# Kernel tuning notes

Hardware: AMD Instinct MI355X
Metric: run time of the kernel (lower is better)

Reference implementation:

```python
import jax, jax.numpy as jnp
import numpy as np
import math

B, S, HID = 2, 2048, 1024
NH, HD = 16, 64
MAX_SEQ = 65536  # RoPE base from RotaryEmbedding


def _rope_tables(seq_len, dim):
    inv_freq = 1.0 / (MAX_SEQ ** (jnp.arange(0, dim, 2, dtype=jnp.float32) / dim))
    t = jnp.arange(seq_len, dtype=jnp.float32)
    freqs = jnp.einsum('i,j->ij', t, inv_freq)          # [S, dim/2]
    emb = jnp.concatenate([freqs, freqs], axis=-1)      # [S, dim]
    return jnp.cos(emb), jnp.sin(emb)


def _rotate_half(x):
    x1, x2 = jnp.split(x, 2, axis=-1)
    return jnp.concatenate([-x2, x1], axis=-1)


def setup_inputs() -> dict:
    key = jax.random.key(0)
    ks = jax.random.split(key, 9)
    std_qkv = 1.0 / math.sqrt(NH * HD)
    std_o = 1.0 / math.sqrt(HID)
    return {
        'input_embeds': jax.random.normal(ks[0], (B, S, HID), dtype=jnp.float32),
        'Wq': jax.random.normal(ks[1], (NH * HD, HID), dtype=jnp.float32) * std_qkv,
        'bq': jnp.zeros((NH * HD,), dtype=jnp.float32),
        'Wk': jax.random.normal(ks[2], (NH * HD, HID), dtype=jnp.float32) * std_qkv,
        'bk': jnp.zeros((NH * HD,), dtype=jnp.float32),
        'Wv': jax.random.normal(ks[3], (NH * HD, HID), dtype=jnp.float32) * std_qkv,
        'bv': jnp.zeros((NH * HD,), dtype=jnp.float32),
        'Wo': jax.random.normal(ks[4], (HID, NH * HD), dtype=jnp.float32) * std_o,
        'bo': jnp.zeros((HID,), dtype=jnp.float32),
    }


def reference(input_embeds, Wq, bq, Wk, bk, Wv, bv, Wo, bo):
    x = input_embeds
    b, s, _ = x.shape
    # QKV projections (torch Linear: x @ W.T + b)
    q = x @ Wq.T + bq
    k = x @ Wk.T + bk
    v = x @ Wv.T + bv
    # [B, S, NH*HD] -> [B, NH, S, HD]
    q = q.reshape(b, s, NH, HD).transpose(0, 2, 1, 3)
    k = k.reshape(b, s, NH, HD).transpose(0, 2, 1, 3)
    v = v.reshape(b, s, NH, HD).transpose(0, 2, 1, 3)
    # RoPE
    cos, sin = _rope_tables(s, HD)  # [S, HD]
    q = q * cos + _rotate_half(q) * sin
    k = k * cos + _rotate_half(k) * sin
    # SDPA (non-causal, no mask)
    scale = 1.0 / math.sqrt(HD)
    scores = jnp.einsum('bhqd,bhkd->bhqk', q, k) * scale
    attn = jax.nn.softmax(scores, axis=-1)
    out = jnp.einsum('bhqk,bhkd->bhqd', attn, v)
    # [B, NH, S, HD] -> [B, S, NH*HD]
    out = out.transpose(0, 2, 1, 3).reshape(b, s, NH * HD)
    return out @ Wo.T + bo
```

## Files before the change

### kernel.cpp

```cpp
#include <hip/hip_runtime.h>
#include <cstdint>
#include <cstddef>

#define S_LEN 2048
#define NHEAD 16
#define HDIM  64
#define HID_  1024

typedef short s8v  __attribute__((ext_vector_type(8)));
typedef short s4v  __attribute__((ext_vector_type(4)));
typedef float f4v  __attribute__((ext_vector_type(4)));
typedef float f16v __attribute__((ext_vector_type(16)));

__device__ __forceinline__ short f2b(float x) {
    union { float f; unsigned u; } a; a.f = x;
    unsigned r = a.u + 0x7fffu + ((a.u >> 16) & 1u);
    return (short)(r >> 16);
}
__device__ __forceinline__ float b2f(short x) {
    union { unsigned u; float f; } a; a.u = ((unsigned)(unsigned short)x) << 16;
    return a.f;
}

__device__ __forceinline__ void gload_lds16(const void* g, void* l) {
    __builtin_amdgcn_global_load_lds(
        (__attribute__((address_space(1))) void*)const_cast<void*>(g),
        (__attribute__((address_space(3))) void*)l, 16, 0, 0);
}

__device__ __forceinline__ unsigned cvtpk(float a, float b) {
    unsigned r;
    asm("v_cvt_pk_bf16_f32 %0, %1, %2" : "=v"(r) : "v"(a), "v"(b));
    return r;
}
__device__ __forceinline__ void plswap(unsigned& a, unsigned& b) {
    asm("v_permlane32_swap_b32 %0, %1" : "+v"(a), "+v"(b));
}

__global__ __launch_bounds__(256) void f2b_kernel(const float* __restrict__ in,
                                                  short* __restrict__ out, int n4) {
    int i = blockIdx.x * 256 + threadIdx.x;
    if (i >= n4) return;
    float4 v = reinterpret_cast<const float4*>(in)[i];
    s4v o;
    o[0] = f2b(v.x); o[1] = f2b(v.y); o[2] = f2b(v.z); o[3] = f2b(v.w);
    reinterpret_cast<s4v*>(out)[i] = o;
}

__global__ __launch_bounds__(256) void f2bw_kernel(
    const float* __restrict__ Wq, const float* __restrict__ Wk,
    const float* __restrict__ Wv, const float* __restrict__ Wo,
    short* __restrict__ Wcat, short* __restrict__ Wob)
{
    const int y = blockIdx.y;
    const float* src = (y == 0) ? Wq : (y == 1) ? Wk : (y == 2) ? Wv : Wo;
    short* dst = (y < 3) ? (Wcat + (size_t)y * 1048576) : Wob;
    int i = blockIdx.x * 256 + threadIdx.x;
    float4 v = reinterpret_cast<const float4*>(src)[i];
    s4v o;
    o[0] = f2b(v.x); o[1] = f2b(v.y); o[2] = f2b(v.z); o[3] = f2b(v.w);
    reinterpret_cast<s4v*>(dst)[i] = o;
}

__global__ __launch_bounds__(256) void rope_table_kernel(float2* __restrict__ tab) {
    int idx = blockIdx.x * 256 + threadIdx.x;
    int s = idx >> 5, j = idx & 31;
    float inv = exp2f(-0.5f * (float)j);
    float ang = (float)s * inv;
    float2 cs; cs.x = cosf(ang); cs.y = sinf(ang);
    tab[idx] = cs;
}

__global__ __launch_bounds__(256) void gemm_qkv(
    const short* __restrict__ A, const short* __restrict__ Bw,
    const float* __restrict__ bq, const float* __restrict__ bk,
    const float* __restrict__ bv,
    short* __restrict__ Qo, short* __restrict__ Ko, short* __restrict__ Vo,
    const float2* __restrict__ rtab)
{
    __shared__ short Asl[2][128 * 32];
    __shared__ short Bsl[2][128 * 32];
    const int t = threadIdx.x;
    const int lane = t & 63;
    const int l15 = lane & 15, l4 = lane >> 4;
    const int wid = t >> 6;
    const int blk = blockIdx.x;
    const int x = blk & 7, j = blk >> 3;
    const int tn = (x * 3 + j % 3) * 128;
    const int tm = (j / 3) * 128;
    const int K = 1024;
    const int wrow = (wid >> 1) * 64, wcol = (wid & 1) * 64;

    f4v acc[4][4];
#pragma unroll
    for (int i = 0; i < 4; ++i)
#pragma unroll
        for (int jj = 0; jj < 4; ++jj) acc[i][jj] = (f4v){0.f, 0.f, 0.f, 0.f};

    const int r0 = t >> 2;
    const int c0 = (t & 3) * 8;
    const int wbase = (t & ~63) * 8;

#define QSTAGE(buf, kt) do { const int k0_ = (kt) << 5;                            \
        gload_lds16(A  + (size_t)(tm + r0)      * K + k0_ + c0, &Asl[buf][wbase]);        \
        gload_lds16(A  + (size_t)(tm + 64 + r0) * K + k0_ + c0, &Asl[buf][2048 + wbase]); \
        gload_lds16(Bw + (size_t)(tn + r0)      * K + k0_ + c0, &Bsl[buf][wbase]);        \
        gload_lds16(Bw + (size_t)(tn + 64 + r0) * K + k0_ + c0, &Bsl[buf][2048 + wbase]); \
    } while (0)

    QSTAGE(0, 0);
    __syncthreads();
    int cur = 0;
    for (int kt = 0; kt < 32; ++kt) {
        if (kt < 31) QSTAGE(cur ^ 1, kt + 1);
        s8v af[4], bf[4];
#pragma unroll
        for (int i = 0; i < 4; ++i) {
            af[i] = *(const s8v*)&Asl[cur][(wrow + i * 16 + l15) * 32 + 8 * l4];
            bf[i] = *(const s8v*)&Bsl[cur][(wcol + i * 16 + l15) * 32 + 8 * l4];
        }
#pragma unroll
        for (int i = 0; i < 4; ++i)
#pragma unroll
            for (int jj = 0; jj < 4; ++jj)
                acc[i][jj] = __builtin_amdgcn_mfma_f32_16x16x32_bf16(af[i], bf[jj], acc[i][jj], 0, 0, 0);
        __syncthreads();
        cur ^= 1;
    }
#undef QSTAGE

    const int mode = tn >> 10;
    const float* bias = (mode == 0) ? bq : (mode == 1) ? bk : bv;
    short* outb = (mode == 0) ? Qo : (mode == 1) ? Ko : Vo;

    if (mode == 2) {
#pragma unroll
        for (int i = 0; i < 4; ++i) {
            int rowb = tm + wrow + i * 16 + l4 * 4;
            int b_ = rowb >> 11, s0 = rowb & 2047;
#pragma unroll
            for (int jj = 0; jj < 4; ++jj) {
                int col = tn + wcol + jj * 16 + l15;
                int cm = col & 1023;
                float bvv = bias[cm];
                int h = cm >> 6, d = col & 63;
                s4v o4;
#pragma unroll
                for (int r = 0; r < 4; ++r) o4[r] = f2b(acc[i][jj][r] + bvv);
                *(s4v*)&outb[((size_t)((b_ * NHEAD + h) * 64 + d)) * S_LEN + s0] = o4;
            }
        }
    } else {
        int h = ((tn & 1023) + wcol) >> 6;
        const float osc = (mode == 0) ? 0.180336880111f : 1.0f;
#pragma unroll
        for (int i = 0; i < 4; ++i) {
#pragma unroll
            for (int r = 0; r < 4; ++r) {
                int row = tm + wrow + i * 16 + l4 * 4 + r;
                int b_ = row >> 11, s = row & 2047;
                float2 cs0 = rtab[(s << 5) + l15];
                float2 cs1 = rtab[(s << 5) + 16 + l15];
#pragma unroll
                for (int jj = 0; jj < 4; ++jj) {
                    int col = tn + wcol + jj * 16 + l15;
                    int cm = col & 1023;
                    int d = col & 63;
                    float v  = acc[i][jj][r]     + bias[cm];
                    float vp = acc[i][jj ^ 2][r] + bias[cm ^ 32];
                    float2 cs = (jj & 1) ? cs1 : cs0;
                    float res = (d < 32) ? (v * cs.x - vp * cs.y)
                                         : (v * cs.x + vp * cs.y);
                    outb[(((size_t)(b_ * NHEAD + h) * S_LEN + s) << 6) + d] = f2b(res * osc);
                }
            }
        }
    }
}

__global__ __launch_bounds__(256) void gemm_o(
    const short* __restrict__ A, const short* __restrict__ Bw,
    const float* __restrict__ bias, float* __restrict__ outf)
{
    __shared__ short Asl[2][64 * 32];
    __shared__ short Bsl[2][128 * 32];
    const int t = threadIdx.x;
    const int lane = t & 63;
    const int l15 = lane & 15, l4 = lane >> 4;
    const int wid = t >> 6;
    const int blk = blockIdx.x;
    const int tn = (blk & 7) * 128;
    const int tm = (blk >> 3) * 64;
    const int K = 1024, N = 1024;
    const int wrow = (wid >> 1) * 32, wcol = (wid & 1) * 64;

    f4v acc[2][4];
#pragma unroll
    for (int i = 0; i < 2; ++i)
#pragma unroll
        for (int jj = 0; jj < 4; ++jj) acc[i][jj] = (f4v){0.f, 0.f, 0.f, 0.f};

    const int r0 = t >> 2;
    const int c0 = (t & 3) * 8;
    const int wbase = (t & ~63) * 8;

#define OSTAGE(buf, kt) do { const int k0_ = (kt) << 5;                            \
        gload_lds16(A  + (size_t)(tm + r0)      * K + k0_ + c0, &Asl[buf][wbase]);        \
        gload_lds16(Bw + (size_t)(tn + r0)      * K + k0_ + c0, &Bsl[buf][wbase]);        \
        gload_lds16(Bw + (size_t)(tn + 64 + r0) * K + k0_ + c0, &Bsl[buf][2048 + wbase]); \
    } while (0)

    OSTAGE(0, 0);
    __syncthreads();
    int cur = 0;
    for (int kt = 0; kt < 32; ++kt) {
        if (kt < 31) OSTAGE(cur ^ 1, kt + 1);
        s8v af[2], bf[4];
#pragma unroll
        for (int i = 0; i < 2; ++i)
            af[i] = *(const s8v*)&Asl[cur][(wrow + i * 16 + l15) * 32 + 8 * l4];
#pragma unroll
        for (int jj = 0; jj < 4; ++jj)
            bf[jj] = *(const s8v*)&Bsl[cur][(wcol + jj * 16 + l15) * 32 + 8 * l4];
#pragma unroll
        for (int i = 0; i < 2; ++i)
#pragma unroll
            for (int jj = 0; jj < 4; ++jj)
                acc[i][jj] = __builtin_amdgcn_mfma_f32_16x16x32_bf16(af[i], bf[jj], acc[i][jj], 0, 0, 0);
        __syncthreads();
        cur ^= 1;
    }
#undef OSTAGE

#pragma unroll
    for (int i = 0; i < 2; ++i) {
        int rowb = tm + wrow + i * 16 + l4 * 4;
#pragma unroll
        for (int jj = 0; jj < 4; ++jj) {
            int col = tn + wcol + jj * 16 + l15;
            float bv = bias[col];
#pragma unroll
            for (int r = 0; r < 4; ++r)
                outf[(size_t)(rowb + r) * N + col] = acc[i][jj][r] + bv;
        }
    }
}

#define SWB(row, bofs) ((bofs) ^ (((row) & 7) << 4))

__global__ __launch_bounds__(256) void attn_split(
    const short* __restrict__ Q, const short* __restrict__ K,
    const short* __restrict__ Vt,
    short* __restrict__ P0, short* __restrict__ P1, float2* __restrict__ ML)
{
    __shared__ short Kl[2][4096];
    __shared__ short Vl[2][4096];

    const int t = threadIdx.x, lane = t & 63, wid = t >> 6;
    const int q5 = lane & 31, hi = lane >> 5;

    const int blk = blockIdx.x;
    const int x = blk & 7, j = blk >> 3;
    const int bh = x * 4 + (j & 3);
    const int rest = j >> 2;
    const int qb = rest & 15, split = rest >> 4;
    const int kt0 = split * 16;

    const short* Qb = Q + (size_t)bh * S_LEN * 64;
    const char*  Kb = (const char*)(K  + (size_t)bh * S_LEN * 64);
    const char*  Vb = (const char*)(Vt + (size_t)bh * S_LEN * 64);
    const int qrow = qb * 128 + wid * 32 + q5;

    s8v qf[4];
#pragma unroll
    for (int sl = 0; sl < 4; ++sl)
        qf[sl] = *(const s8v*)&Qb[(size_t)qrow * 64 + sl * 16 + hi * 8];

    f16v oacc[2];
#pragma unroll
    for (int dt = 0; dt < 2; ++dt)
#pragma unroll
        for (int e = 0; e < 16; ++e) oacc[dt][e] = 0.f;
    float m2 = -1e30f, lsum = 0.f;

    const int skey  = t >> 3;
    const int sboff = (t & 7) * 16;
    const int ssw   = SWB(skey, sboff);
    const size_t koffB = (size_t)skey * 128  + ssw;
    const size_t voffB = (size_t)skey * 4096 + ssw;

#define STAGE(buf, kb) do {                                                        \
        gload_lds16(Kb + (size_t)(kb) * 128 + koffB,              &Kl[buf][wid * 512]);        \
        gload_lds16(Kb + (size_t)(kb) * 128 + koffB + 32 * 128,   &Kl[buf][2048 + wid * 512]); \
        gload_lds16(Vb + (size_t)(kb) * 2   + voffB,              &Vl[buf][wid * 512]);        \
        gload_lds16(Vb + (size_t)(kb) * 2   + voffB + 32 * 4096,  &Vl[buf][2048 + wid * 512]); \
    } while (0)

    STAGE(0, kt0 * 64);
    __syncthreads();

    int cur = 0;
    for (int kt = kt0; kt < kt0 + 16; ++kt) {
        if (kt < kt0 + 15) STAGE(cur ^ 1, (kt + 1) * 64);

        f16v sc[2];
#pragma unroll
        for (int c = 0; c < 2; ++c) {
#pragma unroll
            for (int e = 0; e < 16; ++e) sc[c][e] = 0.f;
            const int krow = c * 32 + q5;
            const char* kbase = (const char*)&Kl[cur][0] + krow * 128;
            __builtin_amdgcn_s_setprio(1);
#pragma unroll
            for (int sl = 0; sl < 4; ++sl) {
                s8v kf = *(const s8v*)(kbase + SWB(krow, sl * 32 + hi * 16));
                sc[c] = __builtin_amdgcn_mfma_f32_32x32x16_bf16(kf, qf[sl], sc[c], 0, 0, 0);
            }
            __builtin_amdgcn_s_setprio(0);
        }

        float pm = -1e30f;
#pragma unroll
        for (int c = 0; c < 2; ++c)
#pragma unroll
            for (int e = 0; e < 16; e += 2)
                pm = fmaxf(pm, fmaxf(sc[c][e], sc[c][e + 1]));
        pm = fmaxf(pm, __shfl_xor(pm, 32, 64));
        if (__any(pm > m2 + 8.0f)) {
            float m2n = fmaxf(m2, pm);
            float fr = __builtin_amdgcn_exp2f(m2 - m2n);
            lsum *= fr;
#pragma unroll
            for (int dt = 0; dt < 2; ++dt)
#pragma unroll
                for (int e = 0; e < 16; ++e) oacc[dt][e] *= fr;
            m2 = m2n;
        }
        float ps = 0.f;
#pragma unroll
        for (int c = 0; c < 2; ++c)
#pragma unroll
            for (int e = 0; e < 16; ++e) {
                float p = __builtin_amdgcn_exp2f(sc[c][e] - m2);
                sc[c][e] = p;
                ps += p;
            }
        lsum += ps;

#pragma unroll
        for (int c = 0; c < 2; ++c) {
#pragma unroll
            for (int ks = 0; ks < 2; ++ks) {
                const int b0 = ks * 8;
                unsigned x0 = cvtpk(sc[c][b0 + 0], sc[c][b0 + 1]);
                unsigned y0 = cvtpk(sc[c][b0 + 4], sc[c][b0 + 5]);
                unsigned x1 = cvtpk(sc[c][b0 + 2], sc[c][b0 + 3]);
                unsigned y1 = cvtpk(sc[c][b0 + 6], sc[c][b0 + 7]);
                plswap(x0, y0);
                plswap(x1, y1);
                union { unsigned u[4]; s8v s; } pf;
                pf.u[0] = x0; pf.u[1] = x1; pf.u[2] = y0; pf.u[3] = y1;
                __builtin_amdgcn_s_setprio(1);
#pragma unroll
                for (int dt = 0; dt < 2; ++dt) {
                    const int vrow = dt * 32 + q5;
                    s8v vf = *(const s8v*)((const char*)&Vl[cur][0] + vrow * 128 +
                                           SWB(vrow, c * 64 + ks * 32 + hi * 16));
                    oacc[dt] = __builtin_amdgcn_mfma_f32_32x32x16_bf16(vf, pf.s, oacc[dt], 0, 0, 0);
                }
                __builtin_amdgcn_s_setprio(0);
            }
        }

        __syncthreads();
        cur ^= 1;
    }

    float ls = lsum + __shfl_xor(lsum, 32, 64);
    float inv = 1.0f / ls;
    short* Pp = (split ? P1 : P0) + ((size_t)bh * S_LEN + qrow) * 64;
#pragma unroll
    for (int dt = 0; dt < 2; ++dt)
#pragma unroll
        for (int g = 0; g < 4; ++g) {
            s4v o4;
#pragma unroll
            for (int jj = 0; jj < 4; ++jj) o4[jj] = f2b(oacc[dt][g * 4 + jj] * inv);
            const int d0 = dt * 32 + g * 8 + hi * 4;
            *(s4v*)&Pp[d0] = o4;
        }
    if (hi == 0) {
        float2 ml; ml.x = m2; ml.y = ls;
        ML[(size_t)split * (32 * S_LEN) + bh * S_LEN + qrow] = ml;
    }
}

__global__ __launch_bounds__(256) void attn_combine(
    const short* __restrict__ P0, const short* __restrict__ P1,
    const float2* __restrict__ ML, short* __restrict__ Obf)
{
    int idx = blockIdx.x * 256 + threadIdx.x;
    int row = idx >> 3;
    int d0 = (idx & 7) * 8;
    float2 a = ML[row];
    float2 b = ML[32 * S_LEN + row];
    float m = fmaxf(a.x, b.x);
    float w0 = a.y * exp2f(a.x - m);
    float w1 = b.y * exp2f(b.x - m);
    float inv = 1.0f / (w0 + w1);
    w0 *= inv; w1 *= inv;
    s8v v0 = *(const s8v*)&P0[(size_t)row * 64 + d0];
    s8v v1 = *(const s8v*)&P1[(size_t)row * 64 + d0];
    s8v o;
#pragma unroll
    for (int e = 0; e < 8; ++e) o[e] = f2b(w0 * b2f(v0[e]) + w1 * b2f(v1[e]));
    int bh = row >> 11, s = row & 2047;
    int b_ = bh >> 4, h = bh & 15;
    *(s8v*)&Obf[((size_t)(b_ * S_LEN + s)) * HID_ + h * 64 + d0] = o;
}

extern "C" void kernel_launch(void* const* d_in, const int* in_sizes, int n_in,
                              void* d_out, int out_size, void* d_ws, size_t ws_size,
                              hipStream_t stream)
{
    const float* X  = (const float*)d_in[0];
    const float* Wq = (const float*)d_in[1];
    const float* bq = (const float*)d_in[2];
    const float* Wk = (const float*)d_in[3];
    const float* bk = (const float*)d_in[4];
    const float* Wv = (const float*)d_in[5];
    const float* bv = (const float*)d_in[6];
    const float* Wo = (const float*)d_in[7];
    const float* bo = (const float*)d_in[8];
    float* out = (float*)d_out;

    char* ws = (char*)d_ws;
    short*  Xb   = (short*) (ws);
    short*  Wcat = (short*) (ws + ( 8u << 20));
    short*  Wob  = (short*) (ws + (14u << 20));
    float2* rtab = (float2*)(ws + (16u << 20));
    short*  Qbh  = (short*) (ws + (17u << 20));
    short*  Kbh  = (short*) (ws + (25u << 20));
    short*  Vbh  = (short*) (ws + (33u << 20));
    short*  Obf  = (short*) (ws + (41u << 20));
    short*  P0   = (short*) (ws);
    short*  P1   = (short*) d_out;
    float2* ML   = (float2*)((char*)d_out + (8u << 20));

    f2b_kernel<<<4096, 256, 0, stream>>>(X, Xb, 1048576);
    f2bw_kernel<<<dim3(1024, 4), 256, 0, stream>>>(Wq, Wk, Wv, Wo, Wcat, Wob);
    rope_table_kernel<<<256, 256, 0, stream>>>(rtab);

    gemm_qkv<<<768, 256, 0, stream>>>(Xb, Wcat, bq, bk, bv, Qbh, Kbh, Vbh, rtab);
    attn_split<<<1024, 256, 0, stream>>>(Qbh, Kbh, Vbh, P0, P1, ML);
    attn_combine<<<2048, 256, 0, stream>>>(P0, P1, ML, Obf);
    gemm_o<<<512, 256, 0, stream>>>(Obf, Wob, bo, out);
}
```

Before: 157.8 us.

## Single-buffer attention LDS with register prefetch and tree reductions

Replaces the double-buffered direct global-to-LDS staging of K/V tiles with a single LDS buffer. The next tile is prefetched into registers, then written to LDS between two barriers. It also sets launch bounds to 4 blocks per SM and rewrites the row max and sum as tree reductions to shorten dependency chains. The aim is to halve LDS use so more blocks fit, at the cost of an extra barrier per iteration and more registers for the prefetch.

```diff
diff --git a/kernel.cpp b/kernel.cpp
--- a/kernel.cpp
+++ b/kernel.cpp
@@ -248,15 +248,16 @@
 
 #define SWB(row, bofs) ((bofs) ^ (((row) & 7) << 4))
 
-__global__ __launch_bounds__(256) void attn_split(
+__global__ __launch_bounds__(256, 4) void attn_split(
     const short* __restrict__ Q, const short* __restrict__ K,
     const short* __restrict__ Vt,
     short* __restrict__ P0, short* __restrict__ P1, float2* __restrict__ ML)
 {
-    __shared__ short Kl[2][4096];
-    __shared__ short Vl[2][4096];
-
-    const int t = threadIdx.x, lane = t & 63, wid = t >> 6;
+    __shared__ short Kl[4096];
+    __shared__ short Vl[4096];
+
+    const int t = threadIdx.x, lane = t & 63;
+    const int wid = t >> 6;
     const int q5 = lane & 31, hi = lane >> 5;
 
     const int blk = blockIdx.x;
@@ -285,23 +286,37 @@
 
     const int skey  = t >> 3;
     const int sboff = (t & 7) * 16;
-    const int ssw   = SWB(skey, sboff);
-    const size_t koffB = (size_t)skey * 128  + ssw;
-    const size_t voffB = (size_t)skey * 4096 + ssw;
-
-#define STAGE(buf, kb) do {                                                        \
-        gload_lds16(Kb + (size_t)(kb) * 128 + koffB,              &Kl[buf][wid * 512]);        \
-        gload_lds16(Kb + (size_t)(kb) * 128 + koffB + 32 * 128,   &Kl[buf][2048 + wid * 512]); \
-        gload_lds16(Vb + (size_t)(kb) * 2   + voffB,              &Vl[buf][wid * 512]);        \
-        gload_lds16(Vb + (size_t)(kb) * 2   + voffB + 32 * 4096,  &Vl[buf][2048 + wid * 512]); \
-    } while (0)
-
-    STAGE(0, kt0 * 64);
+    const int sw    = SWB(skey, sboff);
+    const size_t kgoff = (size_t)skey * 128  + sboff;
+    const size_t vgoff = (size_t)skey * 4096 + sboff;
+    char* KlB = (char*)Kl;
+    char* VlB = (char*)Vl;
+    const int w0 = skey * 128 + sw;
+    const int w1 = w0 + 32 * 128;
+
+    {
+        const size_t kbB = (size_t)kt0 * 64 * 128;
+        const size_t vbB = (size_t)kt0 * 64 * 2;
+        s8v g0 = *(const s8v*)(Kb + kbB + kgoff);
+        s8v g1 = *(const s8v*)(Kb + kbB + kgoff + 32 * 128);
+        s8v g2 = *(const s8v*)(Vb + vbB + vgoff);
+        s8v g3 = *(const s8v*)(Vb + vbB + vgoff + 32 * 4096);
+        *(s8v*)(KlB + w0) = g0; *(s8v*)(KlB + w1) = g1;
+        *(s8v*)(VlB + w0) = g2; *(s8v*)(VlB + w1) = g3;
+    }
     __syncthreads();
 
-    int cur = 0;
     for (int kt = kt0; kt < kt0 + 16; ++kt) {
-        if (kt < kt0 + 15) STAGE(cur ^ 1, (kt + 1) * 64);
+        s8v g0, g1, g2, g3;
+        const bool pre = (kt < kt0 + 15);
+        if (pre) {
+            const size_t kbB = (size_t)(kt + 1) * 64 * 128;
+            const size_t vbB = (size_t)(kt + 1) * 64 * 2;
+            g0 = *(const s8v*)(Kb + kbB + kgoff);
+            g1 = *(const s8v*)(Kb + kbB + kgoff + 32 * 128);
+            g2 = *(const s8v*)(Vb + vbB + vgoff);
+            g3 = *(const s8v*)(Vb + vbB + vgoff + 32 * 4096);
+        }
 
         f16v sc[2];
 #pragma unroll
@@ -309,7 +324,7 @@
 #pragma unroll
             for (int e = 0; e < 16; ++e) sc[c][e] = 0.f;
             const int krow = c * 32 + q5;
-            const char* kbase = (const char*)&Kl[cur][0] + krow * 128;
+            const char* kbase = KlB + krow * 128;
             __builtin_amdgcn_s_setprio(1);
 #pragma unroll
             for (int sl = 0; sl < 4; ++sl) {
@@ -319,12 +334,12 @@
             __builtin_amdgcn_s_setprio(0);
         }
 
-        float pm = -1e30f;
-#pragma unroll
-        for (int c = 0; c < 2; ++c)
-#pragma unroll
-            for (int e = 0; e < 16; e += 2)
-                pm = fmaxf(pm, fmaxf(sc[c][e], sc[c][e + 1]));
+        float m8[8];
+#pragma unroll
+        for (int e = 0; e < 8; ++e)
+            m8[e] = fmaxf(fmaxf(sc[0][e], sc[0][e + 8]), fmaxf(sc[1][e], sc[1][e + 8]));
+        float pm = fmaxf(fmaxf(fmaxf(m8[0], m8[4]), fmaxf(m8[1], m8[5])),
+                         fmaxf(fmaxf(m8[2], m8[6]), fmaxf(m8[3], m8[7])));
         pm = fmaxf(pm, __shfl_xor(pm, 32, 64));
         if (__any(pm > m2 + 8.0f)) {
             float m2n = fmaxf(m2, pm);
@@ -336,16 +351,17 @@
                 for (int e = 0; e < 16; ++e) oacc[dt][e] *= fr;
             m2 = m2n;
         }
-        float ps = 0.f;
 #pragma unroll
         for (int c = 0; c < 2; ++c)
 #pragma unroll
-            for (int e = 0; e < 16; ++e) {
-                float p = __builtin_amdgcn_exp2f(sc[c][e] - m2);
-                sc[c][e] = p;
-                ps += p;
-            }
-        lsum += ps;
+            for (int e = 0; e < 16; ++e)
+                sc[c][e] = __builtin_amdgcn_exp2f(sc[c][e] - m2);
+        float sum8[8];
+#pragma unroll
+        for (int e = 0; e < 8; ++e)
+            sum8[e] = (sc[0][e] + sc[0][e + 8]) + (sc[1][e] + sc[1][e + 8]);
+        lsum += ((sum8[0] + sum8[4]) + (sum8[1] + sum8[5])) +
+                ((sum8[2] + sum8[6]) + (sum8[3] + sum8[7]));
 
 #pragma unroll
         for (int c = 0; c < 2; ++c) {
@@ -364,7 +380,7 @@
 #pragma unroll
                 for (int dt = 0; dt < 2; ++dt) {
                     const int vrow = dt * 32 + q5;
-                    s8v vf = *(const s8v*)((const char*)&Vl[cur][0] + vrow * 128 +
+                    s8v vf = *(const s8v*)(VlB + vrow * 128 +
                                            SWB(vrow, c * 64 + ks * 32 + hi * 16));
                     oacc[dt] = __builtin_amdgcn_mfma_f32_32x32x16_bf16(vf, pf.s, oacc[dt], 0, 0, 0);
                 }
@@ -373,7 +389,11 @@
         }
 
         __syncthreads();
-        cur ^= 1;
+        if (pre) {
+            *(s8v*)(KlB + w0) = g0; *(s8v*)(KlB + w1) = g1;
+            *(s8v*)(VlB + w0) = g2; *(s8v*)(VlB + w1) = g3;
+        }
+        __syncthreads();
     }
 
     float ls = lsum + __shfl_xor(lsum, 32, 64);
```

Result: faster. 153.6 us (-2.7%).
